# Kernel optimization log

Measured on AMD Instinct MI355X. Metric: run time of the kernel, lower is better.

## Reference

```python
import jax, jax.numpy as jnp
import numpy as np
import math

B, N, E, D = 4, 8192, 1024, 64

def setup_inputs() -> dict:
    key = jax.random.key(0)
    kx, kq, kk, kv, ko = jax.random.split(key, 5)
    x = jax.random.normal(kx, (B, N, E), dtype=jnp.float32)
    # ImplicitLinear weights: hash-generated Rademacher-like values scaled by 1/sqrt(in_features).
    # We stand in with sign(normal) * scale, matching the statistics of v_mask_generative * scale.
    wq = jnp.sign(jax.random.normal(kq, (D, E), dtype=jnp.float32)) / math.sqrt(E)
    wk = jnp.sign(jax.random.normal(kk, (D, E), dtype=jnp.float32)) / math.sqrt(E)
    wv = jnp.sign(jax.random.normal(kv, (D, E), dtype=jnp.float32)) / math.sqrt(E)
    wo = jnp.sign(jax.random.normal(ko, (E, D), dtype=jnp.float32)) / math.sqrt(D)
    return {"x": x, "wq": wq, "wk": wk, "wv": wv, "wo": wo}

def reference(x, wq, wk, wv, wo):
    # Projections: ImplicitLinear computes x @ W.T with W shaped [out, in]
    Q = jnp.einsum('bne,de->bnd', x, wq)   # [B,N,D]
    K = jnp.einsum('bne,de->bnd', x, wk)   # [B,N,D]
    V = jnp.einsum('bne,de->bnd', x, wv)   # [B,N,D]
    # ground mode: linear attention, energy = K^T @ V  -> [B,D,D]
    energy = jnp.einsum('bnd,bne->bde', K, V)
    context = jnp.einsum('bnd,bde->bne', Q, energy)  # [B,N,D]
    context = context * jnp.asarray(math.sqrt(3.0 / D), dtype=context.dtype)
    out = jnp.einsum('bnd,ed->bne', context, wo)  # [B,N,E]
    return out
```

## Files before the change

kernel.cpp:

```cpp
#include <hip/hip_runtime.h>
#include <hip/hip_bf16.h>


typedef __bf16 bf16x8 __attribute__((ext_vector_type(8)));
typedef float  f32x4  __attribute__((ext_vector_type(4)));

#define MFMA_BF16(A, Bb, C) __builtin_amdgcn_mfma_f32_16x16x32_bf16(A, Bb, C, 0, 0, 0)

__device__ inline __bf16 bf16_trunc(float v) {
    return __builtin_bit_cast(__bf16, (unsigned short)(__float_as_uint(v) >> 16));
}

__global__ __launch_bounds__(512) void qkv_kernel(
    const float* __restrict__ x,  const float* __restrict__ wq,
    const float* __restrict__ wk, const float* __restrict__ wv,
    float* __restrict__ Qf, float* __restrict__ Kf, float* __restrict__ Vf)
{
    __shared__ __bf16 xh[128 * 64];
    __shared__ __bf16 xl[128 * 64];
    __shared__ __bf16 wl[192 * 64];

    const int tid  = threadIdx.x;
    const int lane = tid & 63;
    const int wid  = tid >> 6;
    const int lr   = lane & 15;
    const int kg   = lane >> 4;
    const int wm   = wid >> 1;
    const int wn   = wid & 1;
    const int row0 = blockIdx.x * 128;

    const int sr = tid >> 2;
    const int sk = (tid & 3) * 16;

    f32x4 acc[2][6];
#pragma unroll
    for (int i = 0; i < 2; ++i)
#pragma unroll
        for (int j = 0; j < 6; ++j) acc[i][j] = (f32x4){0.f, 0.f, 0.f, 0.f};

    for (int step = 0; step < 16; ++step) {
        {
            const float* src = x + (size_t)(row0 + sr) * 1024 + step * 64 + sk;
            float v[16];
            *(float4*)&v[0]  = *(const float4*)(src + 0);
            *(float4*)&v[4]  = *(const float4*)(src + 4);
            *(float4*)&v[8]  = *(const float4*)(src + 8);
            *(float4*)&v[12] = *(const float4*)(src + 12);
            bf16x8 h0, h1, l0, l1;
#pragma unroll
            for (int i = 0; i < 8; ++i) {
                unsigned int b0 = __float_as_uint(v[i]);
                h0[i] = __builtin_bit_cast(__bf16, (unsigned short)(b0 >> 16));
                l0[i] = (__bf16)(v[i] - __uint_as_float(b0 & 0xffff0000u));
                unsigned int b1 = __float_as_uint(v[8 + i]);
                h1[i] = __builtin_bit_cast(__bf16, (unsigned short)(b1 >> 16));
                l1[i] = (__bf16)(v[8 + i] - __uint_as_float(b1 & 0xffff0000u));
            }
            const int s0 = sk >> 3;
            const int p0 = ((s0    ) ^ (sr & 7)) << 3;
            const int p1 = ((s0 + 1) ^ (sr & 7)) << 3;
            *(bf16x8*)&xh[sr * 64 + p0] = h0;
            *(bf16x8*)&xh[sr * 64 + p1] = h1;
            *(bf16x8*)&xl[sr * 64 + p0] = l0;
            *(bf16x8*)&xl[sr * 64 + p1] = l1;
        }
#pragma unroll
        for (int i = 0; i < 3; ++i) {
            const int sid = tid + i * 512;
            const int col = sid >> 3;
            const int sig = sid & 7;
            const int kk  = step * 64 + ((sig ^ (col & 7)) << 3);
            const float* wsrc = (col < 64)  ? (wq + (size_t)col * 1024 + kk)
                              : (col < 128) ? (wk + (size_t)(col - 64) * 1024 + kk)
                                            : (wv + (size_t)(col - 128) * 1024 + kk);
            float w[8];
            *(float4*)&w[0] = *(const float4*)(wsrc + 0);
            *(float4*)&w[4] = *(const float4*)(wsrc + 4);
            bf16x8 wb;
#pragma unroll
            for (int j = 0; j < 8; ++j) wb[j] = bf16_trunc(w[j]);
            *(bf16x8*)&wl[col * 64 + sig * 8] = wb;
        }
        __syncthreads();
#pragma unroll
        for (int ks = 0; ks < 2; ++ks) {
            bf16x8 Ah[2], Al[2], Bw[6];
#pragma unroll
            for (int am = 0; am < 2; ++am) {
                const int row  = wm * 32 + am * 16 + lr;
                const int slot = ks * 4 + kg;
                const int off  = row * 64 + ((slot ^ (row & 7)) << 3);
                Ah[am] = *(const bf16x8*)&xh[off];
                Al[am] = *(const bf16x8*)&xl[off];
            }
#pragma unroll
            for (int bn = 0; bn < 6; ++bn) {
                const int col  = wn * 96 + bn * 16 + lr;
                const int slot = ks * 4 + kg;
                Bw[bn] = *(const bf16x8*)&wl[col * 64 + ((slot ^ (col & 7)) << 3)];
            }
#pragma unroll
            for (int am = 0; am < 2; ++am)
#pragma unroll
                for (int bn = 0; bn < 6; ++bn) {
                    acc[am][bn] = MFMA_BF16(Ah[am], Bw[bn], acc[am][bn]);
                    acc[am][bn] = MFMA_BF16(Al[am], Bw[bn], acc[am][bn]);
                }
        }
        __syncthreads();
    }
#pragma unroll
    for (int am = 0; am < 2; ++am)
#pragma unroll
        for (int bn = 0; bn < 6; ++bn) {
            const int col = wn * 96 + bn * 16 + lr;
            float* dst = (col < 64) ? Qf : (col < 128) ? Kf : Vf;
            const int cc = col & 63;
            const int rb = row0 + wm * 32 + am * 16 + kg * 4;
#pragma unroll
            for (int r = 0; r < 4; ++r)
                dst[(size_t)(rb + r) * 64 + cc] = acc[am][bn][r];
        }
}

__global__ __launch_bounds__(256) void energy_partial_kernel(
    const float* __restrict__ Kf, const float* __restrict__ Vf,
    float* __restrict__ part)
{
    __shared__ float lK[32][64];
    __shared__ float lV[32][64];
    const int tid  = threadIdx.x;
    const int d    = tid >> 2;
    const int e0   = (tid & 3) << 4;
    const int row0 = blockIdx.x * 128;

    float acc[16];
#pragma unroll
    for (int j = 0; j < 16; ++j) acc[j] = 0.f;

    for (int base = 0; base < 128; base += 32) {
        __syncthreads();
#pragma unroll
        for (int i = 0; i < 2; ++i) {
            const int idx = tid + i * 256;
            const int r   = idx >> 4;
            const int c4  = (idx & 15) << 2;
            *(float4*)&lK[r][c4] = *(const float4*)&Kf[(size_t)(row0 + base + r) * 64 + c4];
            *(float4*)&lV[r][c4] = *(const float4*)&Vf[(size_t)(row0 + base + r) * 64 + c4];
        }
        __syncthreads();
        for (int n = 0; n < 32; ++n) {
            const float kv = lK[n][d];
            const float4 a = *(const float4*)&lV[n][e0];
            const float4 b = *(const float4*)&lV[n][e0 + 4];
            const float4 c = *(const float4*)&lV[n][e0 + 8];
            const float4 e = *(const float4*)&lV[n][e0 + 12];
            acc[0]  += kv * a.x; acc[1]  += kv * a.y; acc[2]  += kv * a.z; acc[3]  += kv * a.w;
            acc[4]  += kv * b.x; acc[5]  += kv * b.y; acc[6]  += kv * b.z; acc[7]  += kv * b.w;
            acc[8]  += kv * c.x; acc[9]  += kv * c.y; acc[10] += kv * c.z; acc[11] += kv * c.w;
            acc[12] += kv * e.x; acc[13] += kv * e.y; acc[14] += kv * e.z; acc[15] += kv * e.w;
        }
    }
    float* p = part + (size_t)blockIdx.x * 4096 + d * 64 + e0;
#pragma unroll
    for (int i = 0; i < 4; ++i)
        *(float4*)&p[i * 4] = make_float4(acc[i*4+0], acc[i*4+1], acc[i*4+2], acc[i*4+3]);
}

__global__ __launch_bounds__(256) void energy_reduce_kernel(
    const float* __restrict__ part, float* __restrict__ energy)
{
    const int b    = blockIdx.x >> 4;
    const int elem = ((blockIdx.x & 15) << 8) + threadIdx.x;
    float s = 0.f;
#pragma unroll 8
    for (int c = 0; c < 64; ++c)
        s += part[(size_t)(b * 64 + c) * 4096 + elem];
    energy[b * 4096 + elem] = s;
}

__global__ __launch_bounds__(512) void out_kernel(
    const float* __restrict__ Qf, const float* __restrict__ energy,
    const float* __restrict__ wo, float* __restrict__ out)
{
    __shared__ __align__(16) unsigned char lds[83968];
    __bf16* ctxh = (__bf16*)lds;
    __bf16* ctxl = (__bf16*)(lds + 16384);
    float*  Qs   = (float*)(lds + 32768);
    float*  Es   = (float*)(lds + 32768 + 34816);
    __bf16* wls  = (__bf16*)(lds + 32768);

    const int tid  = threadIdx.x;
    const int lane = tid & 63;
    const int wid  = tid >> 6;
    const int lr   = lane & 15;
    const int kg   = lane >> 4;
    const int row0 = blockIdx.x * 128;
    const int b    = blockIdx.x >> 6;
    const float scale = 0.2165063509461097f;

    {
        const int r  = tid >> 2;
        const int k0 = (tid & 3) << 4;
        const float* src = Qf + (size_t)(row0 + r) * 64 + k0;
#pragma unroll
        for (int i = 0; i < 4; ++i)
            *(float4*)&Qs[r * 68 + k0 + i * 4] = *(const float4*)(src + i * 4);
#pragma unroll
        for (int i = 0; i < 2; ++i) {
            const int idx = (tid + i * 512) << 2;
            float4 ev = *(const float4*)&energy[b * 4096 + idx];
            ev.x *= scale; ev.y *= scale; ev.z *= scale; ev.w *= scale;
            *(float4*)&Es[idx] = ev;
        }
    }
    __syncthreads();
    {
        const int row = tid >> 2;
        const int e0  = (tid & 3) << 4;
        float a[16];
#pragma unroll
        for (int j = 0; j < 16; ++j) a[j] = 0.f;
        for (int dd = 0; dd < 64; ++dd) {
            const float q = Qs[row * 68 + dd];
            const float4 v0 = *(const float4*)&Es[dd * 64 + e0];
            const float4 v1 = *(const float4*)&Es[dd * 64 + e0 + 4];
            const float4 v2 = *(const float4*)&Es[dd * 64 + e0 + 8];
            const float4 v3 = *(const float4*)&Es[dd * 64 + e0 + 12];
            a[0]  += q * v0.x; a[1]  += q * v0.y; a[2]  += q * v0.z; a[3]  += q * v0.w;
            a[4]  += q * v1.x; a[5]  += q * v1.y; a[6]  += q * v1.z; a[7]  += q * v1.w;
            a[8]  += q * v2.x; a[9]  += q * v2.y; a[10] += q * v2.z; a[11] += q * v2.w;
            a[12] += q * v3.x; a[13] += q * v3.y; a[14] += q * v3.z; a[15] += q * v3.w;
        }
        bf16x8 h[2], l[2];
#pragma unroll
        for (int g = 0; g < 2; ++g)
#pragma unroll
            for (int j = 0; j < 8; ++j) {
                const float vv = a[g * 8 + j];
                const unsigned int bb = __float_as_uint(vv);
                h[g][j] = __builtin_bit_cast(__bf16, (unsigned short)(bb >> 16));
                l[g][j] = (__bf16)(vv - __uint_as_float(bb & 0xffff0000u));
            }
        const int s0 = e0 >> 3;
        const int p0 = ((s0    ) ^ (row & 7)) << 3;
        const int p1 = ((s0 + 1) ^ (row & 7)) << 3;
        *(bf16x8*)&ctxh[row * 64 + p0] = h[0];
        *(bf16x8*)&ctxh[row * 64 + p1] = h[1];
        *(bf16x8*)&ctxl[row * 64 + p0] = l[0];
        *(bf16x8*)&ctxl[row * 64 + p1] = l[1];
    }
    __syncthreads();

    const int wm = wid >> 2;
    const int wn = wid & 3;
    for (int nt = 0; nt < 4; ++nt) {
        if (nt) __syncthreads();
#pragma unroll
        for (int i = 0; i < 4; ++i) {
            const int sid = tid + i * 512;
            const int col = sid >> 3;
            const int sig = sid & 7;
            const float* src = wo + (size_t)(nt * 256 + col) * 64 + ((sig ^ (col & 7)) << 3);
            float w[8];
            *(float4*)&w[0] = *(const float4*)(src + 0);
            *(float4*)&w[4] = *(const float4*)(src + 4);
            bf16x8 wb;
#pragma unroll
            for (int j = 0; j < 8; ++j) wb[j] = bf16_trunc(w[j]);
            *(bf16x8*)&wls[col * 64 + sig * 8] = wb;
        }
        __syncthreads();

        f32x4 acc[4][4];
#pragma unroll
        for (int i = 0; i < 4; ++i)
#pragma unroll
            for (int j = 0; j < 4; ++j) acc[i][j] = (f32x4){0.f, 0.f, 0.f, 0.f};

#pragma unroll
        for (int ks = 0; ks < 2; ++ks) {
            bf16x8 Ah[4], Al[4], Bw[4];
#pragma unroll
            for (int am = 0; am < 4; ++am) {
                const int row  = wm * 64 + am * 16 + lr;
                const int slot = ks * 4 + kg;
                const int off  = row * 64 + ((slot ^ (row & 7)) << 3);
                Ah[am] = *(const bf16x8*)&ctxh[off];
                Al[am] = *(const bf16x8*)&ctxl[off];
            }
#pragma unroll
            for (int bn = 0; bn < 4; ++bn) {
                const int col  = wn * 64 + bn * 16 + lr;
                const int slot = ks * 4 + kg;
                Bw[bn] = *(const bf16x8*)&wls[col * 64 + ((slot ^ (col & 7)) << 3)];
            }
#pragma unroll
            for (int am = 0; am < 4; ++am)
#pragma unroll
                for (int bn = 0; bn < 4; ++bn) {
                    acc[am][bn] = MFMA_BF16(Ah[am], Bw[bn], acc[am][bn]);
                    acc[am][bn] = MFMA_BF16(Al[am], Bw[bn], acc[am][bn]);
                }
        }
#pragma unroll
        for (int am = 0; am < 4; ++am)
#pragma unroll
            for (int bn = 0; bn < 4; ++bn) {
                const int gcol = nt * 256 + wn * 64 + bn * 16 + lr;
                const int grow = row0 + wm * 64 + am * 16 + kg * 4;
#pragma unroll
                for (int r = 0; r < 4; ++r)
                    out[(size_t)(grow + r) * 1024 + gcol] = acc[am][bn][r];
            }
    }
}

extern "C" void kernel_launch(void* const* d_in, const int* in_sizes, int n_in,
                              void* d_out, int out_size, void* d_ws, size_t ws_size,
                              hipStream_t stream)
{
    const float* x  = (const float*)d_in[0];
    const float* wq = (const float*)d_in[1];
    const float* wk = (const float*)d_in[2];
    const float* wv = (const float*)d_in[3];
    const float* wo = (const float*)d_in[4];
    float* out = (float*)d_out;

    char* ws = (char*)d_ws;
    float* Qf     = (float*)(ws);
    float* Kf     = (float*)(ws + 8388608);
    float* Vf     = (float*)(ws + 16777216);
    float* part   = (float*)(ws + 25165824);
    float* energy = (float*)(ws + 29360128);

    qkv_kernel<<<256, 512, 0, stream>>>(x, wq, wk, wv, Qf, Kf, Vf);
    energy_partial_kernel<<<256, 256, 0, stream>>>(Kf, Vf, part);
    energy_reduce_kernel<<<64, 256, 0, stream>>>(part, energy);
    out_kernel<<<256, 512, 0, stream>>>(Qf, energy, wo, out);
}
```

Before: 309.2 us.

## Pre-convert weights to bf16, double-buffer QKV with async LDS loads, MFMA context

Adds a prep kernel that converts the QKV and output weights to swizzled bf16 once per call, so the GEMM kernels can load them straight into LDS with global_load_lds and double buffering. The QKV kernel now uses 64-row tiles across 512 blocks and stores Q as split bf16 hi/lo. The out kernel computes Q·energy with MFMA instead of scalar FMAs, reads Wo directly from global memory, and uses nontemporal stores. The energy scale is folded into the reduce kernel. Wt shares workspace with part, which is safe only because qkv finishes reading Wt before energy_partial writes part. Weights are now rounded to bf16 rather than truncated, and the extra kernel launch adds overhead.

```diff
diff --git a/kernel.cpp b/kernel.cpp
--- a/kernel.cpp
+++ b/kernel.cpp
@@ -1,174 +1,222 @@
 #include <hip/hip_runtime.h>
 #include <hip/hip_bf16.h>
+#include <stdint.h>
 
 
 typedef __bf16 bf16x8 __attribute__((ext_vector_type(8)));
+typedef __bf16 bf16x4 __attribute__((ext_vector_type(4)));
 typedef float  f32x4  __attribute__((ext_vector_type(4)));
 
 #define MFMA_BF16(A, Bb, C) __builtin_amdgcn_mfma_f32_16x16x32_bf16(A, Bb, C, 0, 0, 0)
 
-__device__ inline __bf16 bf16_trunc(float v) {
-    return __builtin_bit_cast(__bf16, (unsigned short)(__float_as_uint(v) >> 16));
+__device__ __forceinline__ int swz8(int row, int slot) { return (slot ^ (row & 7)) << 3; }
+
+__device__ __forceinline__ void gload_lds16(const void* g, void* l) {
+    __builtin_amdgcn_global_load_lds(
+        (const __attribute__((address_space(1))) unsigned int*)g,
+        (__attribute__((address_space(3))) unsigned int*)l, 16, 0, 0);
+}
+
+__global__ __launch_bounds__(256) void prep_kernel(
+    const float* __restrict__ wq, const float* __restrict__ wk,
+    const float* __restrict__ wv, const float* __restrict__ wo,
+    __bf16* __restrict__ Wt, __bf16* __restrict__ Wob)
+{
+    const int idx = blockIdx.x * 256 + threadIdx.x;
+    if (idx < 24576) {
+        const int col  = idx >> 7;
+        const int rem  = idx & 127;
+        const int step = rem >> 3;
+        const int slot = rem & 7;
+        const float* src = (col < 64)  ? wq + (size_t)col * 1024
+                         : (col < 128) ? wk + (size_t)(col - 64) * 1024
+                                       : wv + (size_t)(col - 128) * 1024;
+        src += step * 64 + slot * 8;
+        float w[8];
+        *(float4*)&w[0] = *(const float4*)(src);
+        *(float4*)&w[4] = *(const float4*)(src + 4);
+        bf16x8 wb;
+#pragma unroll
+        for (int j = 0; j < 8; ++j) wb[j] = (__bf16)w[j];
+        *(bf16x8*)&Wt[(size_t)step * 12288 + col * 64 + swz8(col, slot)] = wb;
+    } else {
+        const int c2 = idx - 24576;
+        const int e  = c2 >> 3;
+        const int s  = c2 & 7;
+        float w[8];
+        *(float4*)&w[0] = *(const float4*)&wo[(size_t)e * 64 + s * 8];
+        *(float4*)&w[4] = *(const float4*)&wo[(size_t)e * 64 + s * 8 + 4];
+        bf16x8 wb;
+#pragma unroll
+        for (int j = 0; j < 8; ++j) wb[j] = (__bf16)w[j];
+        *(bf16x8*)&Wob[(size_t)e * 64 + s * 8] = wb;
+    }
 }
 
 __global__ __launch_bounds__(512) void qkv_kernel(
-    const float* __restrict__ x,  const float* __restrict__ wq,
-    const float* __restrict__ wk, const float* __restrict__ wv,
-    float* __restrict__ Qf, float* __restrict__ Kf, float* __restrict__ Vf)
-{
-    __shared__ __bf16 xh[128 * 64];
-    __shared__ __bf16 xl[128 * 64];
-    __shared__ __bf16 wl[192 * 64];
+    const float* __restrict__ x, const __bf16* __restrict__ Wt,
+    __bf16* __restrict__ Qh, __bf16* __restrict__ Ql,
+    float* __restrict__ Kf, float* __restrict__ Vf)
+{
+    __shared__ __bf16 xh[64 * 64];
+    __shared__ __bf16 xl[64 * 64];
+    __shared__ __bf16 wl[2][192 * 64];
 
     const int tid  = threadIdx.x;
     const int lane = tid & 63;
     const int wid  = tid >> 6;
     const int lr   = lane & 15;
     const int kg   = lane >> 4;
-    const int wm   = wid >> 1;
-    const int wn   = wid & 1;
-    const int row0 = blockIdx.x * 128;
-
-    const int sr = tid >> 2;
-    const int sk = (tid & 3) * 16;
-
-    f32x4 acc[2][6];
+    const int wm   = wid >> 2;
+    const int wn   = wid & 3;
+    const int row0 = blockIdx.x * 64;
+
+    f32x4 acc[2][3];
 #pragma unroll
     for (int i = 0; i < 2; ++i)
 #pragma unroll
-        for (int j = 0; j < 6; ++j) acc[i][j] = (f32x4){0.f, 0.f, 0.f, 0.f};
+        for (int j = 0; j < 3; ++j) acc[i][j] = (f32x4){0.f, 0.f, 0.f, 0.f};
+
+    float xv[8];
+
+#define STAGE_W(stp, buf)                                                      \
+    {                                                                          \
+        _Pragma("unroll")                                                      \
+        for (int i = 0; i < 3; ++i) {                                          \
+            const int boff = wid * 3072 + i * 1024;                            \
+            gload_lds16((const char*)Wt + (size_t)(stp) * 24576 + boff + (lane << 4), \
+                        (char*)&wl[buf][0] + boff);                            \
+        }                                                                      \
+    }
+#define LOAD_X(stp)                                                            \
+    {                                                                          \
+        _Pragma("unroll")                                                      \
+        for (int i = 0; i < 2; ++i) {                                          \
+            const int s4 = tid + i * 512;                                      \
+            const int r  = s4 >> 4, f4 = s4 & 15;                              \
+            *(float4*)&xv[i * 4] =                                             \
+                *(const float4*)&x[(size_t)(row0 + r) * 1024 + (stp) * 64 + f4 * 4]; \
+        }                                                                      \
+    }
+
+    STAGE_W(0, 0);
+    LOAD_X(0);
 
     for (int step = 0; step < 16; ++step) {
-        {
-            const float* src = x + (size_t)(row0 + sr) * 1024 + step * 64 + sk;
-            float v[16];
-            *(float4*)&v[0]  = *(const float4*)(src + 0);
-            *(float4*)&v[4]  = *(const float4*)(src + 4);
-            *(float4*)&v[8]  = *(const float4*)(src + 8);
-            *(float4*)&v[12] = *(const float4*)(src + 12);
-            bf16x8 h0, h1, l0, l1;
-#pragma unroll
-            for (int i = 0; i < 8; ++i) {
-                unsigned int b0 = __float_as_uint(v[i]);
-                h0[i] = __builtin_bit_cast(__bf16, (unsigned short)(b0 >> 16));
-                l0[i] = (__bf16)(v[i] - __uint_as_float(b0 & 0xffff0000u));
-                unsigned int b1 = __float_as_uint(v[8 + i]);
-                h1[i] = __builtin_bit_cast(__bf16, (unsigned short)(b1 >> 16));
-                l1[i] = (__bf16)(v[8 + i] - __uint_as_float(b1 & 0xffff0000u));
-            }
-            const int s0 = sk >> 3;
-            const int p0 = ((s0    ) ^ (sr & 7)) << 3;
-            const int p1 = ((s0 + 1) ^ (sr & 7)) << 3;
-            *(bf16x8*)&xh[sr * 64 + p0] = h0;
-            *(bf16x8*)&xh[sr * 64 + p1] = h1;
-            *(bf16x8*)&xl[sr * 64 + p0] = l0;
-            *(bf16x8*)&xl[sr * 64 + p1] = l1;
-        }
-#pragma unroll
-        for (int i = 0; i < 3; ++i) {
-            const int sid = tid + i * 512;
-            const int col = sid >> 3;
-            const int sig = sid & 7;
-            const int kk  = step * 64 + ((sig ^ (col & 7)) << 3);
-            const float* wsrc = (col < 64)  ? (wq + (size_t)col * 1024 + kk)
-                              : (col < 128) ? (wk + (size_t)(col - 64) * 1024 + kk)
-                                            : (wv + (size_t)(col - 128) * 1024 + kk);
-            float w[8];
-            *(float4*)&w[0] = *(const float4*)(wsrc + 0);
-            *(float4*)&w[4] = *(const float4*)(wsrc + 4);
-            bf16x8 wb;
-#pragma unroll
-            for (int j = 0; j < 8; ++j) wb[j] = bf16_trunc(w[j]);
-            *(bf16x8*)&wl[col * 64 + sig * 8] = wb;
+        const int cur = step & 1;
+#pragma unroll
+        for (int i = 0; i < 2; ++i) {
+            const int s4 = tid + i * 512;
+            const int r  = s4 >> 4, f4 = s4 & 15;
+            bf16x4 h, l;
+#pragma unroll
+            for (int j = 0; j < 4; ++j) {
+                const float v = xv[i * 4 + j];
+                const unsigned int bb = __float_as_uint(v);
+                h[j] = __builtin_bit_cast(__bf16, (unsigned short)(bb >> 16));
+                l[j] = (__bf16)(v - __uint_as_float(bb & 0xffff0000u));
+            }
+            const int off = r * 64 + swz8(r, f4 >> 1) + (f4 & 1) * 4;
+            *(bf16x4*)&xh[off] = h;
+            *(bf16x4*)&xl[off] = l;
         }
         __syncthreads();
+        if (step < 15) {
+            STAGE_W(step + 1, cur ^ 1);
+            LOAD_X(step + 1);
+        }
 #pragma unroll
         for (int ks = 0; ks < 2; ++ks) {
-            bf16x8 Ah[2], Al[2], Bw[6];
+            const int slot = ks * 4 + kg;
+            bf16x8 Ah[2], Al[2], Bw[3];
 #pragma unroll
             for (int am = 0; am < 2; ++am) {
-                const int row  = wm * 32 + am * 16 + lr;
-                const int slot = ks * 4 + kg;
-                const int off  = row * 64 + ((slot ^ (row & 7)) << 3);
-                Ah[am] = *(const bf16x8*)&xh[off];
-                Al[am] = *(const bf16x8*)&xl[off];
-            }
-#pragma unroll
-            for (int bn = 0; bn < 6; ++bn) {
-                const int col  = wn * 96 + bn * 16 + lr;
-                const int slot = ks * 4 + kg;
-                Bw[bn] = *(const bf16x8*)&wl[col * 64 + ((slot ^ (col & 7)) << 3)];
+                const int row = wm * 32 + am * 16 + lr;
+                Ah[am] = *(const bf16x8*)&xh[row * 64 + swz8(row, slot)];
+                Al[am] = *(const bf16x8*)&xl[row * 64 + swz8(row, slot)];
+            }
+#pragma unroll
+            for (int bn = 0; bn < 3; ++bn) {
+                const int col = wn * 48 + bn * 16 + lr;
+                Bw[bn] = *(const bf16x8*)&wl[cur][col * 64 + swz8(col, slot)];
             }
 #pragma unroll
             for (int am = 0; am < 2; ++am)
 #pragma unroll
-                for (int bn = 0; bn < 6; ++bn) {
+                for (int bn = 0; bn < 3; ++bn) {
                     acc[am][bn] = MFMA_BF16(Ah[am], Bw[bn], acc[am][bn]);
                     acc[am][bn] = MFMA_BF16(Al[am], Bw[bn], acc[am][bn]);
                 }
         }
         __syncthreads();
     }
+#undef STAGE_W
+#undef LOAD_X
+
 #pragma unroll
     for (int am = 0; am < 2; ++am)
 #pragma unroll
-        for (int bn = 0; bn < 6; ++bn) {
-            const int col = wn * 96 + bn * 16 + lr;
-            float* dst = (col < 64) ? Qf : (col < 128) ? Kf : Vf;
-            const int cc = col & 63;
-            const int rb = row0 + wm * 32 + am * 16 + kg * 4;
-#pragma unroll
-            for (int r = 0; r < 4; ++r)
-                dst[(size_t)(rb + r) * 64 + cc] = acc[am][bn][r];
-        }
-}
-
-__global__ __launch_bounds__(256) void energy_partial_kernel(
+        for (int bn = 0; bn < 3; ++bn) {
+            const int col  = wn * 48 + bn * 16 + lr;
+            const int rowb = row0 + wm * 32 + am * 16 + kg * 4;
+            if (col < 64) {
+#pragma unroll
+                for (int r = 0; r < 4; ++r) {
+                    const int n   = rowb + r;
+                    const float v = acc[am][bn][r];
+                    const __bf16 h = (__bf16)v;
+                    const __bf16 l = (__bf16)(v - (float)h);
+                    const size_t o = (size_t)n * 64 + swz8(n, col >> 3) + (col & 7);
+                    Qh[o] = h; Ql[o] = l;
+                }
+            } else if (col < 128) {
+#pragma unroll
+                for (int r = 0; r < 4; ++r)
+                    Kf[(size_t)(rowb + r) * 64 + (col - 64)] = acc[am][bn][r];
+            } else {
+#pragma unroll
+                for (int r = 0; r < 4; ++r)
+                    Vf[(size_t)(rowb + r) * 64 + (col - 128)] = acc[am][bn][r];
+            }
+        }
+}
+
+__global__ __launch_bounds__(512) void energy_partial_kernel(
     const float* __restrict__ Kf, const float* __restrict__ Vf,
     float* __restrict__ part)
 {
-    __shared__ float lK[32][64];
-    __shared__ float lV[32][64];
+    __shared__ float lK[32 * 64];
+    __shared__ float lV[32 * 64];
     const int tid  = threadIdx.x;
-    const int d    = tid >> 2;
-    const int e0   = (tid & 3) << 4;
+    const int lane = tid & 63;
+    const int wid  = tid >> 6;
+    const int d    = tid >> 3;
+    const int e0   = (tid & 7) * 8;
     const int row0 = blockIdx.x * 128;
 
-    float acc[16];
-#pragma unroll
-    for (int j = 0; j < 16; ++j) acc[j] = 0.f;
-
-    for (int base = 0; base < 128; base += 32) {
-        __syncthreads();
-#pragma unroll
-        for (int i = 0; i < 2; ++i) {
-            const int idx = tid + i * 256;
-            const int r   = idx >> 4;
-            const int c4  = (idx & 15) << 2;
-            *(float4*)&lK[r][c4] = *(const float4*)&Kf[(size_t)(row0 + base + r) * 64 + c4];
-            *(float4*)&lV[r][c4] = *(const float4*)&Vf[(size_t)(row0 + base + r) * 64 + c4];
-        }
+    float acc[8] = {0.f, 0.f, 0.f, 0.f, 0.f, 0.f, 0.f, 0.f};
+
+    for (int c = 0; c < 4; ++c) {
+        const size_t boff = (size_t)(row0 + c * 32) * 256 + wid * 1024 + (lane << 4);
+        gload_lds16((const char*)Kf + boff, (char*)lK + wid * 1024);
+        gload_lds16((const char*)Vf + boff, (char*)lV + wid * 1024);
         __syncthreads();
         for (int n = 0; n < 32; ++n) {
-            const float kv = lK[n][d];
-            const float4 a = *(const float4*)&lV[n][e0];
-            const float4 b = *(const float4*)&lV[n][e0 + 4];
-            const float4 c = *(const float4*)&lV[n][e0 + 8];
-            const float4 e = *(const float4*)&lV[n][e0 + 12];
-            acc[0]  += kv * a.x; acc[1]  += kv * a.y; acc[2]  += kv * a.z; acc[3]  += kv * a.w;
-            acc[4]  += kv * b.x; acc[5]  += kv * b.y; acc[6]  += kv * b.z; acc[7]  += kv * b.w;
-            acc[8]  += kv * c.x; acc[9]  += kv * c.y; acc[10] += kv * c.z; acc[11] += kv * c.w;
-            acc[12] += kv * e.x; acc[13] += kv * e.y; acc[14] += kv * e.z; acc[15] += kv * e.w;
-        }
+            const float kv = lK[n * 64 + d];
+            const float4 a = *(const float4*)&lV[n * 64 + e0];
+            const float4 b = *(const float4*)&lV[n * 64 + e0 + 4];
+            acc[0] += kv * a.x; acc[1] += kv * a.y; acc[2] += kv * a.z; acc[3] += kv * a.w;
+            acc[4] += kv * b.x; acc[5] += kv * b.y; acc[6] += kv * b.z; acc[7] += kv * b.w;
+        }
+        __syncthreads();
     }
     float* p = part + (size_t)blockIdx.x * 4096 + d * 64 + e0;
-#pragma unroll
-    for (int i = 0; i < 4; ++i)
-        *(float4*)&p[i * 4] = make_float4(acc[i*4+0], acc[i*4+1], acc[i*4+2], acc[i*4+3]);
+    *(float4*)&p[0] = make_float4(acc[0], acc[1], acc[2], acc[3]);
+    *(float4*)&p[4] = make_float4(acc[4], acc[5], acc[6], acc[7]);
 }
 
 __global__ __launch_bounds__(256) void energy_reduce_kernel(
-    const float* __restrict__ part, float* __restrict__ energy)
+    const float* __restrict__ part, __bf16* __restrict__ Eth, __bf16* __restrict__ Etl)
 {
     const int b    = blockIdx.x >> 4;
     const int elem = ((blockIdx.x & 15) << 8) + threadIdx.x;
@@ -176,142 +224,116 @@
 #pragma unroll 8
     for (int c = 0; c < 64; ++c)
         s += part[(size_t)(b * 64 + c) * 4096 + elem];
-    energy[b * 4096 + elem] = s;
+    s *= 0.2165063509461097f;
+    const int d = elem >> 6, e = elem & 63;
+    const __bf16 h = (__bf16)s;
+    const __bf16 l = (__bf16)(s - (float)h);
+    const size_t o = (size_t)b * 4096 + e * 64 + swz8(e, d >> 3) + (d & 7);
+    Eth[o] = h; Etl[o] = l;
 }
 
 __global__ __launch_bounds__(512) void out_kernel(
-    const float* __restrict__ Qf, const float* __restrict__ energy,
-    const float* __restrict__ wo, float* __restrict__ out)
-{
-    __shared__ __align__(16) unsigned char lds[83968];
-    __bf16* ctxh = (__bf16*)lds;
-    __bf16* ctxl = (__bf16*)(lds + 16384);
-    float*  Qs   = (float*)(lds + 32768);
-    float*  Es   = (float*)(lds + 32768 + 34816);
-    __bf16* wls  = (__bf16*)(lds + 32768);
+    const __bf16* __restrict__ Qh, const __bf16* __restrict__ Ql,
+    const __bf16* __restrict__ Eth, const __bf16* __restrict__ Etl,
+    const __bf16* __restrict__ Wob, float* __restrict__ out)
+{
+    __shared__ __bf16 qh[64 * 64];
+    __shared__ __bf16 ql[64 * 64];
+    __shared__ __bf16 ch[64 * 64];
+    __shared__ __bf16 cl[64 * 64];
 
     const int tid  = threadIdx.x;
     const int lane = tid & 63;
     const int wid  = tid >> 6;
     const int lr   = lane & 15;
     const int kg   = lane >> 4;
-    const int row0 = blockIdx.x * 128;
-    const int b    = blockIdx.x >> 6;
-    const float scale = 0.2165063509461097f;
-
-    {
-        const int r  = tid >> 2;
-        const int k0 = (tid & 3) << 4;
-        const float* src = Qf + (size_t)(row0 + r) * 64 + k0;
-#pragma unroll
-        for (int i = 0; i < 4; ++i)
-            *(float4*)&Qs[r * 68 + k0 + i * 4] = *(const float4*)(src + i * 4);
-#pragma unroll
-        for (int i = 0; i < 2; ++i) {
-            const int idx = (tid + i * 512) << 2;
-            float4 ev = *(const float4*)&energy[b * 4096 + idx];
-            ev.x *= scale; ev.y *= scale; ev.z *= scale; ev.w *= scale;
-            *(float4*)&Es[idx] = ev;
-        }
-    }
+    const int wm   = wid >> 2;
+    const int wn   = wid & 3;
+    const int row0 = blockIdx.x * 64;
+    const int b    = blockIdx.x >> 7;
+
+    gload_lds16((const char*)Qh + (size_t)row0 * 128 + wid * 1024 + (lane << 4),
+                (char*)qh + wid * 1024);
+    gload_lds16((const char*)Ql + (size_t)row0 * 128 + wid * 1024 + (lane << 4),
+                (char*)ql + wid * 1024);
     __syncthreads();
-    {
-        const int row = tid >> 2;
-        const int e0  = (tid & 3) << 4;
-        float a[16];
-#pragma unroll
-        for (int j = 0; j < 16; ++j) a[j] = 0.f;
-        for (int dd = 0; dd < 64; ++dd) {
-            const float q = Qs[row * 68 + dd];
-            const float4 v0 = *(const float4*)&Es[dd * 64 + e0];
-            const float4 v1 = *(const float4*)&Es[dd * 64 + e0 + 4];
-            const float4 v2 = *(const float4*)&Es[dd * 64 + e0 + 8];
-            const float4 v3 = *(const float4*)&Es[dd * 64 + e0 + 12];
-            a[0]  += q * v0.x; a[1]  += q * v0.y; a[2]  += q * v0.z; a[3]  += q * v0.w;
-            a[4]  += q * v1.x; a[5]  += q * v1.y; a[6]  += q * v1.z; a[7]  += q * v1.w;
-            a[8]  += q * v2.x; a[9]  += q * v2.y; a[10] += q * v2.z; a[11] += q * v2.w;
-            a[12] += q * v3.x; a[13] += q * v3.y; a[14] += q * v3.z; a[15] += q * v3.w;
-        }
-        bf16x8 h[2], l[2];
-#pragma unroll
-        for (int g = 0; g < 2; ++g)
-#pragma unroll
-            for (int j = 0; j < 8; ++j) {
-                const float vv = a[g * 8 + j];
-                const unsigned int bb = __float_as_uint(vv);
-                h[g][j] = __builtin_bit_cast(__bf16, (unsigned short)(bb >> 16));
-                l[g][j] = (__bf16)(vv - __uint_as_float(bb & 0xffff0000u));
-            }
-        const int s0 = e0 >> 3;
-        const int p0 = ((s0    ) ^ (row & 7)) << 3;
-        const int p1 = ((s0 + 1) ^ (row & 7)) << 3;
-        *(bf16x8*)&ctxh[row * 64 + p0] = h[0];
-        *(bf16x8*)&ctxh[row * 64 + p1] = h[1];
-        *(bf16x8*)&ctxl[row * 64 + p0] = l[0];
-        *(bf16x8*)&ctxl[row * 64 + p1] = l[1];
-    }
+
+    f32x4 cacc[2];
+    cacc[0] = (f32x4){0.f, 0.f, 0.f, 0.f};
+    cacc[1] = (f32x4){0.f, 0.f, 0.f, 0.f};
+#pragma unroll
+    for (int ks = 0; ks < 2; ++ks) {
+        const int slot = ks * 4 + kg;
+        const int e    = wn * 16 + lr;
+        const bf16x8 Bh = *(const bf16x8*)&Eth[(size_t)b * 4096 + e * 64 + swz8(e, slot)];
+        const bf16x8 Bl = *(const bf16x8*)&Etl[(size_t)b * 4096 + e * 64 + swz8(e, slot)];
+#pragma unroll
+        for (int am = 0; am < 2; ++am) {
+            const int row = wm * 32 + am * 16 + lr;
+            const bf16x8 Ah = *(const bf16x8*)&qh[row * 64 + swz8(row, slot)];
+            const bf16x8 Al = *(const bf16x8*)&ql[row * 64 + swz8(row, slot)];
+            cacc[am] = MFMA_BF16(Ah, Bh, cacc[am]);
+            cacc[am] = MFMA_BF16(Ah, Bl, cacc[am]);
+            cacc[am] = MFMA_BF16(Al, Bh, cacc[am]);
+        }
+    }
+#pragma unroll
+    for (int am = 0; am < 2; ++am)
+#pragma unroll
+        for (int r = 0; r < 4; ++r) {
+            const int n = wm * 32 + am * 16 + kg * 4 + r;
+            const int dd = wn * 16 + lr;
+            const float v  = cacc[am][r];
+            const __bf16 h = (__bf16)v;
+            const __bf16 l = (__bf16)(v - (float)h);
+            const int off = n * 64 + swz8(n, dd >> 3) + (dd & 7);
+            ch[off] = h; cl[off] = l;
+        }
     __syncthreads();
 
-    const int wm = wid >> 2;
-    const int wn = wid & 3;
-    for (int nt = 0; nt < 4; ++nt) {
-        if (nt) __syncthreads();
-#pragma unroll
-        for (int i = 0; i < 4; ++i) {
-            const int sid = tid + i * 512;
-            const int col = sid >> 3;
-            const int sig = sid & 7;
-            const float* src = wo + (size_t)(nt * 256 + col) * 64 + ((sig ^ (col & 7)) << 3);
-            float w[8];
-            *(float4*)&w[0] = *(const float4*)(src + 0);
-            *(float4*)&w[4] = *(const float4*)(src + 4);
-            bf16x8 wb;
-#pragma unroll
-            for (int j = 0; j < 8; ++j) wb[j] = bf16_trunc(w[j]);
-            *(bf16x8*)&wls[col * 64 + sig * 8] = wb;
-        }
-        __syncthreads();
-
-        f32x4 acc[4][4];
-#pragma unroll
-        for (int i = 0; i < 4; ++i)
-#pragma unroll
-            for (int j = 0; j < 4; ++j) acc[i][j] = (f32x4){0.f, 0.f, 0.f, 0.f};
-
+    bf16x8 Ah[2][2], Al[2][2];
+#pragma unroll
+    for (int am = 0; am < 2; ++am)
 #pragma unroll
         for (int ks = 0; ks < 2; ++ks) {
-            bf16x8 Ah[4], Al[4], Bw[4];
-#pragma unroll
-            for (int am = 0; am < 4; ++am) {
-                const int row  = wm * 64 + am * 16 + lr;
-                const int slot = ks * 4 + kg;
-                const int off  = row * 64 + ((slot ^ (row & 7)) << 3);
-                Ah[am] = *(const bf16x8*)&ctxh[off];
-                Al[am] = *(const bf16x8*)&ctxl[off];
-            }
+            const int row  = wm * 32 + am * 16 + lr;
+            const int slot = ks * 4 + kg;
+            Ah[am][ks] = *(const bf16x8*)&ch[row * 64 + swz8(row, slot)];
+            Al[am][ks] = *(const bf16x8*)&cl[row * 64 + swz8(row, slot)];
+        }
+#pragma unroll
+    for (int g = 0; g < 4; ++g) {
+        f32x4 oacc[2][4];
+#pragma unroll
+        for (int i = 0; i < 2; ++i)
+#pragma unroll
+            for (int j = 0; j < 4; ++j) oacc[i][j] = (f32x4){0.f, 0.f, 0.f, 0.f};
+#pragma unroll
+        for (int ks = 0; ks < 2; ++ks) {
+            bf16x8 Bw[4];
 #pragma unroll
             for (int bn = 0; bn < 4; ++bn) {
-                const int col  = wn * 64 + bn * 16 + lr;
-                const int slot = ks * 4 + kg;
-                Bw[bn] = *(const bf16x8*)&wls[col * 64 + ((slot ^ (col & 7)) << 3)];
-            }
-#pragma unroll
-            for (int am = 0; am < 4; ++am)
+                const int col = wn * 256 + g * 64 + bn * 16 + lr;
+                Bw[bn] = *(const bf16x8*)&Wob[(size_t)col * 64 + ks * 32 + kg * 8];
+            }
+#pragma unroll
+            for (int am = 0; am < 2; ++am)
 #pragma unroll
                 for (int bn = 0; bn < 4; ++bn) {
-                    acc[am][bn] = MFMA_BF16(Ah[am], Bw[bn], acc[am][bn]);
-                    acc[am][bn] = MFMA_BF16(Al[am], Bw[bn], acc[am][bn]);
+                    oacc[am][bn] = MFMA_BF16(Ah[am][ks], Bw[bn], oacc[am][bn]);
+                    oacc[am][bn] = MFMA_BF16(Al[am][ks], Bw[bn], oacc[am][bn]);
                 }
         }
 #pragma unroll
-        for (int am = 0; am < 4; ++am)
+        for (int am = 0; am < 2; ++am)
 #pragma unroll
             for (int bn = 0; bn < 4; ++bn) {
-                const int gcol = nt * 256 + wn * 64 + bn * 16 + lr;
-                const int grow = row0 + wm * 64 + am * 16 + kg * 4;
+                const int gcol = wn * 256 + g * 64 + bn * 16 + lr;
+                const int grow = row0 + wm * 32 + am * 16 + kg * 4;
 #pragma unroll
                 for (int r = 0; r < 4; ++r)
-                    out[(size_t)(grow + r) * 1024 + gcol] = acc[am][bn][r];
+                    __builtin_nontemporal_store(oacc[am][bn][r],
+                        &out[(size_t)(grow + r) * 1024 + gcol]);
             }
     }
 }
@@ -328,14 +350,19 @@
     float* out = (float*)d_out;
 
     char* ws = (char*)d_ws;
-    float* Qf     = (float*)(ws);
-    float* Kf     = (float*)(ws + 8388608);
-    float* Vf     = (float*)(ws + 16777216);
-    float* part   = (float*)(ws + 25165824);
-    float* energy = (float*)(ws + 29360128);
-
-    qkv_kernel<<<256, 512, 0, stream>>>(x, wq, wk, wv, Qf, Kf, Vf);
-    energy_partial_kernel<<<256, 256, 0, stream>>>(Kf, Vf, part);
-    energy_reduce_kernel<<<64, 256, 0, stream>>>(part, energy);
-    out_kernel<<<256, 512, 0, stream>>>(Qf, energy, wo, out);
-}
+    __bf16* Qh   = (__bf16*)(ws);
+    __bf16* Ql   = (__bf16*)(ws + 4194304);
+    float*  Kf   = (float*)(ws + 8388608);
+    float*  Vf   = (float*)(ws + 16777216);
+    float*  part = (float*)(ws + 25165824);
+    __bf16* Wt   = (__bf16*)(ws + 25165824);
+    __bf16* Eth  = (__bf16*)(ws + 29360128);
+    __bf16* Etl  = (__bf16*)(ws + 29392896);
+    __bf16* Wob  = (__bf16*)(ws + 29425664);
+
+    prep_kernel<<<128, 256, 0, stream>>>(wq, wk, wv, wo, Wt, Wob);
+    qkv_kernel<<<512, 512, 0, stream>>>(x, Wt, Qh, Ql, Kf, Vf);
+    energy_partial_kernel<<<256, 512, 0, stream>>>(Kf, Vf, part);
+    energy_reduce_kernel<<<64, 256, 0, stream>>>(part, Eth, Etl);
+    out_kernel<<<512, 512, 0, stream>>>(Qh, Ql, Eth, Etl, Wob, out);
+}
```

Measured after the change: 293.5 us. -5.1%, faster.
